# Optimization experiments

Measured on AMD Instinct MI355X. Metric: run time of the kernel, lower is better.

## Reference

```python
import jax, jax.numpy as jnp
import numpy as np

EPS = 1e-8
N_IN, N = 1024, 2048


def _signs():
    # torch picks c1, c2 uniformly from {-1, +1} each call; we use a fixed key
    # so the reference is deterministic.
    r = jax.random.randint(jax.random.key(1234), (2,), 0, 2)
    return (2.0 * r.astype(jnp.float32) - 1.0)


def setup_inputs() -> dict:
    key = jax.random.key(0)
    ks = jax.random.split(key, 6)
    x = jax.random.normal(ks[0], (N_IN,), jnp.float32)
    h_prev = jnp.zeros((N,), jnp.float32)  # module buffer starts at zeros
    W_in = jax.random.uniform(ks[1], (N_IN, N), jnp.float32, -0.1, 0.1)
    W_h = jax.random.uniform(ks[2], (N, N), jnp.float32, -0.1, 0.1)
    bias = jax.random.uniform(ks[3], (N,), jnp.float32, -0.1, 0.1)
    u_prev = jax.random.normal(ks[4], (N_IN + N + 1,), jnp.float32)
    A_prev = jax.random.normal(ks[5], (N, N), jnp.float32)
    return {"x": x, "h_prev": h_prev, "W_in": W_in, "W_h": W_h,
            "bias": bias, "u_prev": u_prev, "A_prev": A_prev}


def reference(x, h_prev, W_in, W_h, bias, u_prev, A_prev):
    n = W_h.shape[0]
    z = x @ W_in + h_prev @ W_h + bias          # [n]
    h_next = jnp.tanh(z)
    dh_dz = 1.0 - h_next * h_next               # [n]
    # diag(dh_dz) @ W_h rewritten as a row-wise broadcast scale (same math)
    H = dh_dz[:, None] * W_h                    # [n, n]
    H_q = H @ A_prev                            # [n, n]
    h_q = jnp.concatenate([x, h_prev, jnp.ones((1,), x.dtype)])  # [n_in+n+1]
    c1, c2 = _signs()
    # ||D||_F == ||dh_dz||_2 since D is diagonal
    p1 = jnp.sqrt(jnp.linalg.norm(H_q) / (EPS + jnp.linalg.norm(u_prev)))
    p2 = jnp.sqrt(jnp.linalg.norm(dh_dz) / (EPS + jnp.linalg.norm(h_q)))
    u_next = c1 * p1 * u_prev + c2 * p2 * h_q
    idx = jnp.arange(n)
    A_next = (c1 / (p1 + EPS)) * H_q
    A_next = A_next.at[idx, idx].add((c2 / (p2 + EPS)) * dh_dz)
    # torch Function returns only h_next; u_next/A_next are forward-computed
    # state saved for backward -- returned here so the work is observable.
    return h_next, u_next, A_next
```

## Files before the change

### kernel.cpp

```cpp
#include <hip/hip_runtime.h>
#include <hip/hip_bf16.h>
#include <math.h>

#define C1 1.0f
#define C2 1.0f

static constexpr float EPSF = 1e-8f;
static constexpr int NIN = 1024;
static constexpr int NH  = 2048;
static constexpr int NU  = NIN + NH + 1;

typedef __attribute__((ext_vector_type(8))) short bf16x8;
typedef __attribute__((ext_vector_type(4))) float f32x4;


__device__ inline unsigned short f2bf(float f) {
  union { float f; unsigned u; } v; v.f = f;
  unsigned r = v.u + 0x7FFFu + ((v.u >> 16) & 1u);
  return (unsigned short)(r >> 16);
}

__device__ inline float blockReduce256(float v, float* red) {
  int t = threadIdx.x;
  red[t] = v;
  __syncthreads();
  for (int s = 128; s > 0; s >>= 1) {
    if (t < s) red[t] += red[t + s];
    __syncthreads();
  }
  float r = red[0];
  __syncthreads();
  return r;
}

__global__ void k_stage1(const float* __restrict__ x, const float* __restrict__ hprev,
                         const float* __restrict__ Win, const float* __restrict__ Wh,
                         float* __restrict__ part,
                         const float* __restrict__ Ap, unsigned short* __restrict__ Bt,
                         const float* __restrict__ u, float* __restrict__ nrm) {
  __shared__ float ls[64][65];
  __shared__ float hl[48];
  __shared__ int   idxl[48];
  __shared__ int   cntS;
  int b = blockIdx.x;
  int t = threadIdx.x;
  if (b < 128) {
    int bj = b & 1, bi = b >> 1;
    int jc4 = bj * 256 + t;
    int i0 = bi * 48;
    if (t < 48) {
      int i = i0 + t;
      hl[t] = (i < NIN) ? x[i] : hprev[i - NIN];
    }
    __syncthreads();
    if (t < 64) {
      bool nz = (t < 48) && (hl[t] != 0.0f);
      unsigned long long mask = __ballot(nz);
      if (nz) {
        int pos = __popcll(mask & ((1ull << t) - 1ull));
        idxl[pos] = t;
      }
      if (t == 0) cntS = __popcll(mask);
    }
    __syncthreads();
    int cnt = cntS;
    float4 s = {0.f, 0.f, 0.f, 0.f};
    for (int ii = 0; ii < cnt; ++ii) {
      int rl = idxl[ii];
      int i = i0 + rl;
      const float4* wrow = (i < NIN)
        ? (const float4*)Win + (size_t)i * 512
        : (const float4*)Wh  + (size_t)(i - NIN) * 512;
      float4 w = wrow[jc4];
      float cv = hl[rl];
      s.x += cv * w.x; s.y += cv * w.y; s.z += cv * w.z; s.w += cv * w.w;
    }
    ((float4*)part)[bi * 512 + jc4] = s;
  } else if (b < 1152) {
    int bb = b - 128;
    int tn = bb & 31, tk = bb >> 5;
    int r = t >> 4, c = (t & 15) * 4;
#pragma unroll
    for (int i = 0; i < 4; ++i) {
      float4 v = *(const float4*)&Ap[(size_t)(tk * 64 + r + i * 16) * NH + tn * 64 + c];
      ls[r + i * 16][c] = v.x; ls[r + i * 16][c + 1] = v.y;
      ls[r + i * 16][c + 2] = v.z; ls[r + i * 16][c + 3] = v.w;
    }
    __syncthreads();
#pragma unroll
    for (int i = 0; i < 4; ++i) {
      int n = r + i * 16;
      ushort4 o;
      o.x = f2bf(ls[c][n]);     o.y = f2bf(ls[c + 1][n]);
      o.z = f2bf(ls[c + 2][n]); o.w = f2bf(ls[c + 3][n]);
      *(ushort4*)&Bt[(size_t)(tn * 64 + n) * NH + tk * 64 + c] = o;
    }
  } else {
    float* red = (float*)ls;
    float su = 0, sx = 0, sh = 0;
    for (int i = t; i < NU;  i += 256) su += u[i] * u[i];
    for (int i = t; i < NIN; i += 256) sx += x[i] * x[i];
    for (int i = t; i < NH;  i += 256) sh += hprev[i] * hprev[i];
    float r0 = blockReduce256(su, red);
    float r1 = blockReduce256(sx, red);
    float r2 = blockReduce256(sh, red);
    if (t == 0) { nrm[0] = r0; nrm[1] = r1; nrm[2] = r2; }
  }
}

__global__ void k_prep(const float* __restrict__ Wh, const float* __restrict__ part,
                       const float* __restrict__ bias,
                       unsigned short* __restrict__ Abf,
                       float* __restrict__ outh, float* __restrict__ dh,
                       float* __restrict__ dhp) {
  __shared__ float red[256];
  __shared__ float dhs;
  int b = blockIdx.x, t = threadIdx.x;
  if (b < 4096) {
    int r = b >> 1;
    if (t < 64) red[t] = part[t * NH + r];
    __syncthreads();
    if (t == 0) {
      float z = bias[r];
      for (int i = 0; i < 64; ++i) z += red[i];
      float h = tanhf(z);
      dhs = 1.f - h * h;
    }
    __syncthreads();
    float d = dhs;
    int idx4 = b * 256 + t;
    float4 w = ((const float4*)Wh)[idx4];
    ushort4 o;
    o.x = f2bf(w.x * d); o.y = f2bf(w.y * d);
    o.z = f2bf(w.z * d); o.w = f2bf(w.w * d);
    ((ushort4*)Abf)[idx4] = o;
  } else {
    int j = (b - 4096) * 256 + t;
    float z = bias[j];
    for (int bi = 0; bi < 64; ++bi) z += part[bi * NH + j];
    float h = tanhf(z);
    outh[j] = h;
    float d = 1.f - h * h;
    dh[j] = d;
    float s = blockReduce256(d * d, red);
    if (t == 0) dhp[b - 4096] = s;
  }
}

#define GLOAD_LDS(gsrc, ldst) \
  __builtin_amdgcn_global_load_lds( \
      (const __attribute__((address_space(1))) unsigned int*)(gsrc), \
      (__attribute__((address_space(3))) unsigned int*)(ldst), 16, 0, 0)

__global__ __launch_bounds__(256) void k_gemm(const unsigned short* __restrict__ Abf,
                                              const unsigned short* __restrict__ Bt,
                                              float* __restrict__ Hq,
                                              float* __restrict__ gp) {
  __shared__ unsigned short As[512 * 8];
  __shared__ unsigned short Bs[512 * 8];
  __shared__ float red[256];
  const int K = NH;
  int t = threadIdx.x;
  int lane = t & 63;
  int bid = blockIdx.x;
  int swz = (bid & 7) * 128 + (bid >> 3);
  int bm = swz >> 5, bn = swz & 31;
  int wid = t >> 6;
  int wr = wid >> 1, wc = wid & 1;

  int srow = t >> 3, skg = t & 7;
  int sxg = skg ^ (srow & 7);
  const unsigned short* AgBase = Abf + (size_t)(bm * 64 + srow) * K + sxg * 8;
  const unsigned short* BgBase = Bt  + (size_t)(bn * 64 + srow) * K + sxg * 8;

  f32x4 acc[2][2] = {};

  for (int k0 = 0; k0 < K; k0 += 64) {
    GLOAD_LDS(AgBase + k0,          As + t * 8);
    GLOAD_LDS(AgBase + 32 * K + k0, As + (t + 256) * 8);
    GLOAD_LDS(BgBase + k0,          Bs + t * 8);
    GLOAD_LDS(BgBase + 32 * K + k0, Bs + (t + 256) * 8);
    __syncthreads();
    __builtin_amdgcn_s_setprio(1);
#pragma unroll
    for (int kk = 0; kk < 2; ++kk) {
      bf16x8 af[2], bfr[2];
#pragma unroll
      for (int mi = 0; mi < 2; ++mi) {
        int row = wr * 32 + mi * 16 + (lane & 15);
        int kg = (kk * 4 + (lane >> 4)) ^ (row & 7);
        af[mi] = *(const bf16x8*)&As[(row * 8 + kg) * 8];
      }
#pragma unroll
      for (int ni = 0; ni < 2; ++ni) {
        int row = wc * 32 + ni * 16 + (lane & 15);
        int kg = (kk * 4 + (lane >> 4)) ^ (row & 7);
        bfr[ni] = *(const bf16x8*)&Bs[(row * 8 + kg) * 8];
      }
#pragma unroll
      for (int mi = 0; mi < 2; ++mi)
#pragma unroll
        for (int ni = 0; ni < 2; ++ni)
          acc[mi][ni] = __builtin_amdgcn_mfma_f32_16x16x32_bf16(af[mi], bfr[ni], acc[mi][ni], 0, 0, 0);
    }
    __builtin_amdgcn_s_setprio(0);
    __syncthreads();
  }

  float ss = 0.f;
  int r0 = bm * 64 + wr * 32 + (lane >> 4) * 4;
  int c0 = bn * 64 + wc * 32 + (lane & 15);
#pragma unroll
  for (int mi = 0; mi < 2; ++mi)
#pragma unroll
    for (int r = 0; r < 4; ++r) {
      int row = r0 + mi * 16 + r;
#pragma unroll
      for (int ni = 0; ni < 2; ++ni) {
        float v = acc[mi][ni][r];
        Hq[(size_t)row * NH + c0 + ni * 16] = v;
        ss += v * v;
      }
    }
  float s = blockReduce256(ss, red);
  if (t == 0) gp[blockIdx.x] = s;
}

__global__ void k_Au(float* __restrict__ Hq, const float* __restrict__ dh,
                     const float* __restrict__ gp, const float* __restrict__ dhp,
                     const float* __restrict__ nrm,
                     const float* __restrict__ u, const float* __restrict__ x,
                     const float* __restrict__ hprev, float* __restrict__ outu) {
  __shared__ float red[256];
  __shared__ float cf[4];
  int t = threadIdx.x;
  float s = blockReduce256(gp[t] + gp[t + 256] + gp[t + 512] + gp[t + 768], red);
  if (t == 0) {
    float sdh = 0;
    for (int i = 0; i < 8; ++i) sdh += dhp[i];
    float nu  = sqrtf(nrm[0]);
    float nhq = sqrtf(nrm[1] + nrm[2] + 1.0f);
    float ndh = sqrtf(sdh);
    float nHq = sqrtf(s);
    float p1 = sqrtf(nHq / (EPSF + nu));
    float p2 = sqrtf(ndh / (EPSF + nhq));
    cf[0] = C1 * p1;
    cf[1] = C2 * p2;
    cf[2] = C1 / (p1 + EPSF);
    cf[3] = C2 / (p2 + EPSF);
  }
  __syncthreads();

  if (blockIdx.x >= 2048) {
    int i = (blockIdx.x - 2048) * 256 + t;
    if (i < NU) {
      float hq = (i < NIN) ? x[i] : (i < NIN + NH ? hprev[i - NIN] : 1.0f);
      outu[i] = cf[0] * u[i] + cf[1] * hq;
    }
    return;
  }
  float sA = cf[2], sD = cf[3];
  float4* H4 = (float4*)Hq;
  int i4 = blockIdx.x * 256 + t;
#pragma unroll
  for (int it = 0; it < 2; ++it, i4 += 2048 * 256) {
    float4 v = H4[i4];
    v.x *= sA; v.y *= sA; v.z *= sA; v.w *= sA;
    int row = i4 >> 9;
    int c = (i4 & 511) * 4;
    int j = row - c;
    if (j >= 0 && j < 4) {
      float add = sD * dh[row];
      if (j == 0) v.x += add; else if (j == 1) v.y += add;
      else if (j == 2) v.z += add; else v.w += add;
    }
    H4[i4] = v;
  }
}

extern "C" void kernel_launch(void* const* d_in, const int* in_sizes, int n_in,
                              void* d_out, int out_size, void* d_ws, size_t ws_size,
                              hipStream_t stream) {
  const float* x     = (const float*)d_in[0];
  const float* hprev = (const float*)d_in[1];
  const float* Win   = (const float*)d_in[2];
  const float* Wh    = (const float*)d_in[3];
  const float* bias  = (const float*)d_in[4];
  const float* uprev = (const float*)d_in[5];
  const float* Ap    = (const float*)d_in[6];

  float* out  = (float*)d_out;
  float* outh = out;
  float* outu = out + NH;
  float* Hq   = out + NH + NU;
  float* part = Hq;

  char* ws = (char*)d_ws;
  float* dh   = (float*)ws;
  float* dhp  = (float*)(ws + 8192);
  float* gp   = (float*)(ws + 8256);
  float* nrm  = (float*)(ws + 12352);
  unsigned short* Abf = (unsigned short*)(ws + 16384);
  unsigned short* Bt  = (unsigned short*)(ws + 8404992);

  k_stage1 <<<1153, 256, 0, stream>>>(x, hprev, Win, Wh, part, Ap, Bt, uprev, nrm);
  k_prep   <<<4104, 256, 0, stream>>>(Wh, part, bias, Abf, outh, dh, dhp);
  k_gemm   <<<1024, 256, 0, stream>>>(Abf, Bt, Hq, gp);
  k_Au     <<<2061, 256, 0, stream>>>(Hq, dh, gp, dhp, nrm, uprev, x, hprev, outu);
}
```

Before: 61.13 us.

## Double-buffer LDS tiles in bf16 GEMM to overlap global loads with MFMA

The GEMM k-loop now uses two LDS buffers for the A and B tiles. The next tile is issued via global_load_lds before computing on the current one, with explicit vmcnt waits and raw barriers replacing __syncthreads. This is meant to hide global memory latency behind MFMA work. It doubles LDS use per block, which may reduce occupancy, and it relies on correct manual waitcnt counts.

Result: no change. 61.79 us (+1.1%).

```diff
diff --git a/kernel.cpp b/kernel.cpp
--- a/kernel.cpp
+++ b/kernel.cpp
@@ -156,8 +156,8 @@
                                               const unsigned short* __restrict__ Bt,
                                               float* __restrict__ Hq,
                                               float* __restrict__ gp) {
-  __shared__ unsigned short As[512 * 8];
-  __shared__ unsigned short Bs[512 * 8];
+  __shared__ unsigned short As[2][4096];
+  __shared__ unsigned short Bs[2][4096];
   __shared__ float red[256];
   const int K = NH;
   int t = threadIdx.x;
@@ -173,14 +173,27 @@
   const unsigned short* AgBase = Abf + (size_t)(bm * 64 + srow) * K + sxg * 8;
   const unsigned short* BgBase = Bt  + (size_t)(bn * 64 + srow) * K + sxg * 8;
 
+#define STAGE(buf, k0)                                                  \
+  do {                                                                  \
+    GLOAD_LDS(AgBase + (k0),          &As[buf][0] + t * 8);             \
+    GLOAD_LDS(AgBase + 32 * K + (k0), &As[buf][0] + (t + 256) * 8);     \
+    GLOAD_LDS(BgBase + (k0),          &Bs[buf][0] + t * 8);             \
+    GLOAD_LDS(BgBase + 32 * K + (k0), &Bs[buf][0] + (t + 256) * 8);     \
+  } while (0)
+
   f32x4 acc[2][2] = {};
 
-  for (int k0 = 0; k0 < K; k0 += 64) {
-    GLOAD_LDS(AgBase + k0,          As + t * 8);
-    GLOAD_LDS(AgBase + 32 * K + k0, As + (t + 256) * 8);
-    GLOAD_LDS(BgBase + k0,          Bs + t * 8);
-    GLOAD_LDS(BgBase + 32 * K + k0, Bs + (t + 256) * 8);
-    __syncthreads();
+  STAGE(0, 0);
+  int buf = 0;
+  for (int tt = 0; tt < 32; ++tt) {
+    if (tt < 31) {
+      STAGE(buf ^ 1, (tt + 1) * 64);
+      asm volatile("s_waitcnt vmcnt(4)" ::: "memory");
+    } else {
+      asm volatile("s_waitcnt vmcnt(0)" ::: "memory");
+    }
+    __builtin_amdgcn_s_barrier();
+    __builtin_amdgcn_sched_barrier(0);
     __builtin_amdgcn_s_setprio(1);
 #pragma unroll
     for (int kk = 0; kk < 2; ++kk) {
@@ -189,13 +202,13 @@
       for (int mi = 0; mi < 2; ++mi) {
         int row = wr * 32 + mi * 16 + (lane & 15);
         int kg = (kk * 4 + (lane >> 4)) ^ (row & 7);
-        af[mi] = *(const bf16x8*)&As[(row * 8 + kg) * 8];
+        af[mi] = *(const bf16x8*)&As[buf][(row * 8 + kg) * 8];
       }
 #pragma unroll
       for (int ni = 0; ni < 2; ++ni) {
         int row = wc * 32 + ni * 16 + (lane & 15);
         int kg = (kk * 4 + (lane >> 4)) ^ (row & 7);
-        bfr[ni] = *(const bf16x8*)&Bs[(row * 8 + kg) * 8];
+        bfr[ni] = *(const bf16x8*)&Bs[buf][(row * 8 + kg) * 8];
       }
 #pragma unroll
       for (int mi = 0; mi < 2; ++mi)
@@ -204,8 +217,11 @@
           acc[mi][ni] = __builtin_amdgcn_mfma_f32_16x16x32_bf16(af[mi], bfr[ni], acc[mi][ni], 0, 0, 0);
     }
     __builtin_amdgcn_s_setprio(0);
-    __syncthreads();
-  }
+    asm volatile("s_waitcnt lgkmcnt(0)" ::: "memory");
+    __builtin_amdgcn_s_barrier();
+    buf ^= 1;
+  }
+#undef STAGE
 
   float ss = 0.f;
   int r0 = bm * 64 + wr * 32 + (lane >> 4) * 4;
```
